# Performance work log

Hardware: AMD Instinct MI355X
Metric: run time of the kernel (lower is better)

The kernel has to match this reference:

```python
import jax, jax.numpy as jnp
import numpy as np

B, C, H, W = 256, 3, 224, 224

def setup_inputs() -> dict:
    key = jax.random.key(0)
    k = jax.random.split(key, 6)
    x = jax.random.normal(k[0], (B, C, H, W), dtype=jnp.float32)
    flip_mask = jax.random.uniform(k[1], (B,)) > 0.5
    gray_mask = jax.random.uniform(k[2], (B,)) < 0.2
    brightness = (0.8 + 0.4 * jax.random.uniform(k[3], (B,))).astype(jnp.float32)
    contrast_apply = jax.random.uniform(k[4], (B,)) < 0.5
    contrast_factor = (0.8 + 0.4 * jax.random.uniform(k[5], (B,))).astype(jnp.float32)
    return {
        "x": x,
        "brightness": brightness,
        "contrast_factor": contrast_factor,
        "flip_mask": flip_mask,
        "gray_mask": gray_mask,
        "contrast_apply": contrast_apply,
    }

def reference(x, brightness, contrast_factor, flip_mask, gray_mask, contrast_apply):
    # 1) random horizontal flip (flip last spatial dim) per sample
    fm = flip_mask[:, None, None, None]
    x = jnp.where(fm, x[..., ::-1], x)
    # 2) random grayscale: luma broadcast back to all 3 channels
    gray_w = jnp.asarray([0.2989, 0.587, 0.114], dtype=x.dtype)
    gray = jnp.einsum('c,bchw->bhw', gray_w, x)  # [B,H,W]
    x = jnp.where(gray_mask[:, None, None, None], gray[:, None, :, :], x)
    # 3) per-sample brightness in [0.8, 1.2]
    x = x * brightness[:, None, None, None]
    mean = jnp.mean(x, axis=(2, 3), keepdims=True)  # [B,C,1,1]
    x_contrast = (x - mean) * contrast_factor[:, None, None, None] + mean
    x = jnp.where(contrast_apply[:, None, None, None], x_contrast, x)
    # 5) clamp
    return jnp.clip(x, -2.5, 2.5)
```

## Files before the change

### kernel.cpp

```cpp
#include <hip/hip_runtime.h>

namespace {

constexpr int B_ = 256, C_ = 3, H_ = 224, W_ = 224;
constexpr int HW   = H_ * W_;
constexpr int HW4  = HW / 4;
constexpr int W4   = W_ / 4;
constexpr int BLK  = 256;
constexpr int BLOCKS_PER_IMG = HW4 / BLK;

using f4 = __attribute__((ext_vector_type(4))) float;

__device__ __forceinline__ f4 rev4(f4 v) {
    f4 r; r.x = v.w; r.y = v.z; r.z = v.y; r.w = v.x; return r;
}
__device__ __forceinline__ float clip1(float v) {
    return fminf(fmaxf(v, -2.5f), 2.5f);
}

__global__ __launch_bounds__(BLK) void mean_kernel(const float* __restrict__ x,
                                                   const int* __restrict__ contrast_apply,
                                                   float* __restrict__ means) {
    const int plane = blockIdx.x;
    if (contrast_apply[plane / 3] == 0) {
        if (threadIdx.x == 0) means[plane] = 0.f;
        return;
    }
    const f4* p = reinterpret_cast<const f4*>(x) + (size_t)plane * HW4;

    float s = 0.f;
#pragma unroll 4
    for (int i = threadIdx.x; i < HW4; i += BLK) {
        f4 v = p[i];
        s += (v.x + v.y) + (v.z + v.w);
    }
#pragma unroll
    for (int off = 32; off > 0; off >>= 1) s += __shfl_down(s, off, 64);

    __shared__ float partial[BLK / 64];
    const int lane = threadIdx.x & 63;
    const int wv   = threadIdx.x >> 6;
    if (lane == 0) partial[wv] = s;
    __syncthreads();
    if (threadIdx.x == 0) {
        float t = (partial[0] + partial[1]) + (partial[2] + partial[3]);
        means[plane] = t * (1.0f / HW);
    }
}

__global__ __launch_bounds__(BLK) void xform_kernel(
    const float* __restrict__ x,
    const float* __restrict__ brightness,
    const float* __restrict__ cfac,
    const int*  __restrict__ flip_mask,
    const int*  __restrict__ gray_mask,
    const int*  __restrict__ contrast_apply,
    const float* __restrict__ means,
    float* __restrict__ out) {

    const int b = blockIdx.x / BLOCKS_PER_IMG;
    const int p = (blockIdx.x % BLOCKS_PER_IMG) * BLK + threadIdx.x;
    const int h  = p / W4;
    const int w4 = p % W4;

    const bool fl = flip_mask[b] != 0;
    const bool gr = gray_mask[b] != 0;
    const bool ca = contrast_apply[b] != 0;
    const float br = brightness[b];
    const float cf = cfac[b];

    const float m0 = means[b * 3 + 0];
    const float m1 = means[b * 3 + 1];
    const float m2 = means[b * 3 + 2];
    const float gmean = 0.2989f * m0 + 0.587f * m1 + 0.114f * m2;

    const float A = br * (ca ? cf : 1.f);
    float B0 = 0.f, B1 = 0.f, B2 = 0.f;
    if (ca) {
        const float k = br * (1.f - cf);
        if (gr) { B0 = B1 = B2 = k * gmean; }
        else    { B0 = k * m0; B1 = k * m1; B2 = k * m2; }
    }

    const int srcw4 = fl ? (W4 - 1 - w4) : w4;
    const size_t src = (size_t)b * (C_ * HW) + (size_t)h * W_ + (size_t)srcw4 * 4;

    f4 r  = __builtin_nontemporal_load(reinterpret_cast<const f4*>(x + src));
    f4 g  = __builtin_nontemporal_load(reinterpret_cast<const f4*>(x + src + HW));
    f4 bl = __builtin_nontemporal_load(reinterpret_cast<const f4*>(x + src + 2 * HW));
    if (fl) { r = rev4(r); g = rev4(g); bl = rev4(bl); }

    if (gr) {
        f4 gy;
        gy.x = 0.2989f * r.x + 0.587f * g.x + 0.114f * bl.x;
        gy.y = 0.2989f * r.y + 0.587f * g.y + 0.114f * bl.y;
        gy.z = 0.2989f * r.z + 0.587f * g.z + 0.114f * bl.z;
        gy.w = 0.2989f * r.w + 0.587f * g.w + 0.114f * bl.w;
        r = gy; g = gy; bl = gy;
    }

    f4 o0, o1, o2;
    o0.x = clip1(r.x * A + B0);  o0.y = clip1(r.y * A + B0);
    o0.z = clip1(r.z * A + B0);  o0.w = clip1(r.w * A + B0);
    o1.x = clip1(g.x * A + B1);  o1.y = clip1(g.y * A + B1);
    o1.z = clip1(g.z * A + B1);  o1.w = clip1(g.w * A + B1);
    o2.x = clip1(bl.x * A + B2); o2.y = clip1(bl.y * A + B2);
    o2.z = clip1(bl.z * A + B2); o2.w = clip1(bl.w * A + B2);

    const size_t dst = (size_t)b * (C_ * HW) + (size_t)h * W_ + (size_t)w4 * 4;
    __builtin_nontemporal_store(o0, reinterpret_cast<f4*>(out + dst));
    __builtin_nontemporal_store(o1, reinterpret_cast<f4*>(out + dst + HW));
    __builtin_nontemporal_store(o2, reinterpret_cast<f4*>(out + dst + 2 * HW));
}

}

extern "C" void kernel_launch(void* const* d_in, const int* in_sizes, int n_in,
                              void* d_out, int out_size, void* d_ws, size_t ws_size,
                              hipStream_t stream) {
    const float* x          = (const float*)d_in[0];
    const float* brightness = (const float*)d_in[1];
    const float* cfac       = (const float*)d_in[2];
    const int*   flip_mask  = (const int*)d_in[3];
    const int*   gray_mask  = (const int*)d_in[4];
    const int*   contrast_a = (const int*)d_in[5];
    float* out   = (float*)d_out;
    float* means = (float*)d_ws;

    mean_kernel<<<B_ * C_, BLK, 0, stream>>>(x, contrast_a, means);
    xform_kernel<<<B_ * BLOCKS_PER_IMG, BLK, 0, stream>>>(
        x, brightness, cfac, flip_mask, gray_mask, contrast_a, means, out);
}
```

Before: 276.5 us.

## Overlap mean reduction with non-contrast image transforms in a fused launch

The mean reduction is merged into the same launch as the transform for images that don't need contrast, so those images are processed while the reductions run. A second kernel then handles only the contrast images once their means are ready. The goal is to remove the serialization where every image waited on the mean pass. The cost is an extra kernel, since the second launch is full-sized and most of its blocks exit early, plus some branching.

```diff
diff --git a/kernel.cpp b/kernel.cpp
--- a/kernel.cpp
+++ b/kernel.cpp
@@ -8,6 +8,7 @@
 constexpr int W4   = W_ / 4;
 constexpr int BLK  = 256;
 constexpr int BLOCKS_PER_IMG = HW4 / BLK;
+constexpr int NPLANES = B_ * C_;
 
 using f4 = __attribute__((ext_vector_type(4))) float;
 
@@ -18,68 +19,36 @@
     return fminf(fmaxf(v, -2.5f), 2.5f);
 }
 
-__global__ __launch_bounds__(BLK) void mean_kernel(const float* __restrict__ x,
-                                                   const int* __restrict__ contrast_apply,
-                                                   float* __restrict__ means) {
-    const int plane = blockIdx.x;
-    if (contrast_apply[plane / 3] == 0) {
-        if (threadIdx.x == 0) means[plane] = 0.f;
-        return;
-    }
-    const f4* p = reinterpret_cast<const f4*>(x) + (size_t)plane * HW4;
+template <bool ApplyContrast>
+__device__ __forceinline__ void xform_tile(
+    const float* __restrict__ x, float* __restrict__ out,
+    int b, int p,
+    const float* __restrict__ brightness, const float* __restrict__ cfac,
+    const int* __restrict__ flip_mask, const int* __restrict__ gray_mask,
+    const float* __restrict__ means) {
 
-    float s = 0.f;
-#pragma unroll 4
-    for (int i = threadIdx.x; i < HW4; i += BLK) {
-        f4 v = p[i];
-        s += (v.x + v.y) + (v.z + v.w);
-    }
-#pragma unroll
-    for (int off = 32; off > 0; off >>= 1) s += __shfl_down(s, off, 64);
-
-    __shared__ float partial[BLK / 64];
-    const int lane = threadIdx.x & 63;
-    const int wv   = threadIdx.x >> 6;
-    if (lane == 0) partial[wv] = s;
-    __syncthreads();
-    if (threadIdx.x == 0) {
-        float t = (partial[0] + partial[1]) + (partial[2] + partial[3]);
-        means[plane] = t * (1.0f / HW);
-    }
-}
-
-__global__ __launch_bounds__(BLK) void xform_kernel(
-    const float* __restrict__ x,
-    const float* __restrict__ brightness,
-    const float* __restrict__ cfac,
-    const int*  __restrict__ flip_mask,
-    const int*  __restrict__ gray_mask,
-    const int*  __restrict__ contrast_apply,
-    const float* __restrict__ means,
-    float* __restrict__ out) {
-
-    const int b = blockIdx.x / BLOCKS_PER_IMG;
-    const int p = (blockIdx.x % BLOCKS_PER_IMG) * BLK + threadIdx.x;
     const int h  = p / W4;
     const int w4 = p % W4;
 
     const bool fl = flip_mask[b] != 0;
     const bool gr = gray_mask[b] != 0;
-    const bool ca = contrast_apply[b] != 0;
     const float br = brightness[b];
-    const float cf = cfac[b];
 
-    const float m0 = means[b * 3 + 0];
-    const float m1 = means[b * 3 + 1];
-    const float m2 = means[b * 3 + 2];
-    const float gmean = 0.2989f * m0 + 0.587f * m1 + 0.114f * m2;
-
-    const float A = br * (ca ? cf : 1.f);
+    float A = br;
     float B0 = 0.f, B1 = 0.f, B2 = 0.f;
-    if (ca) {
+    if constexpr (ApplyContrast) {
+        const float cf = cfac[b];
+        const float m0 = means[b * 3 + 0];
+        const float m1 = means[b * 3 + 1];
+        const float m2 = means[b * 3 + 2];
+        A = br * cf;
         const float k = br * (1.f - cf);
-        if (gr) { B0 = B1 = B2 = k * gmean; }
-        else    { B0 = k * m0; B1 = k * m1; B2 = k * m2; }
+        if (gr) {
+            const float gm = 0.2989f * m0 + 0.587f * m1 + 0.114f * m2;
+            B0 = B1 = B2 = k * gm;
+        } else {
+            B0 = k * m0; B1 = k * m1; B2 = k * m2;
+        }
     }
 
     const int srcw4 = fl ? (W4 - 1 - w4) : w4;
@@ -113,6 +82,66 @@
     __builtin_nontemporal_store(o2, reinterpret_cast<f4*>(out + dst + 2 * HW));
 }
 
+__global__ __launch_bounds__(BLK) void fusedA_kernel(
+    const float* __restrict__ x,
+    const float* __restrict__ brightness,
+    const int*  __restrict__ flip_mask,
+    const int*  __restrict__ gray_mask,
+    const int*  __restrict__ contrast_apply,
+    float* __restrict__ means,
+    float* __restrict__ out) {
+
+    if (blockIdx.x < NPLANES) {
+        const int plane = blockIdx.x;
+        if (contrast_apply[plane / 3] == 0) {
+            if (threadIdx.x == 0) means[plane] = 0.f;
+            return;
+        }
+        const f4* p = reinterpret_cast<const f4*>(x) + (size_t)plane * HW4;
+        float s = 0.f;
+#pragma unroll 4
+        for (int i = threadIdx.x; i < HW4; i += BLK) {
+            f4 v = p[i];
+            s += (v.x + v.y) + (v.z + v.w);
+        }
+#pragma unroll
+        for (int off = 32; off > 0; off >>= 1) s += __shfl_down(s, off, 64);
+
+        __shared__ float partial[BLK / 64];
+        if ((threadIdx.x & 63) == 0) partial[threadIdx.x >> 6] = s;
+        __syncthreads();
+        if (threadIdx.x == 0) {
+            float t = (partial[0] + partial[1]) + (partial[2] + partial[3]);
+            means[plane] = t * (1.0f / HW);
+        }
+        return;
+    }
+
+    const int idx = blockIdx.x - NPLANES;
+    const int b = idx / BLOCKS_PER_IMG;
+    if (contrast_apply[b] != 0) return;
+    const int p = (idx % BLOCKS_PER_IMG) * BLK + threadIdx.x;
+    xform_tile<false>(x, out, b, p, brightness, nullptr, flip_mask, gray_mask,
+                      nullptr);
+}
+
+__global__ __launch_bounds__(BLK) void xformC_kernel(
+    const float* __restrict__ x,
+    const float* __restrict__ brightness,
+    const float* __restrict__ cfac,
+    const int*  __restrict__ flip_mask,
+    const int*  __restrict__ gray_mask,
+    const int*  __restrict__ contrast_apply,
+    const float* __restrict__ means,
+    float* __restrict__ out) {
+
+    const int b = blockIdx.x / BLOCKS_PER_IMG;
+    if (contrast_apply[b] == 0) return;
+    const int p = (blockIdx.x % BLOCKS_PER_IMG) * BLK + threadIdx.x;
+    xform_tile<true>(x, out, b, p, brightness, cfac, flip_mask, gray_mask,
+                     means);
+}
+
 }
 
 extern "C" void kernel_launch(void* const* d_in, const int* in_sizes, int n_in,
@@ -127,7 +156,8 @@
     float* out   = (float*)d_out;
     float* means = (float*)d_ws;
 
-    mean_kernel<<<B_ * C_, BLK, 0, stream>>>(x, contrast_a, means);
-    xform_kernel<<<B_ * BLOCKS_PER_IMG, BLK, 0, stream>>>(
+    fusedA_kernel<<<NPLANES + B_ * BLOCKS_PER_IMG, BLK, 0, stream>>>(
+        x, brightness, flip_mask, gray_mask, contrast_a, means, out);
+    xformC_kernel<<<B_ * BLOCKS_PER_IMG, BLK, 0, stream>>>(
         x, brightness, cfac, flip_mask, gray_mask, contrast_a, means, out);
 }
```

Measured after the change: 282.1 us. 2.0% more time.
